# Kernel tuning notes

Hardware: AMD Instinct MI355X
Metric: run time of the kernel (lower is better)

The kernel has to match this reference:

```python
import jax, jax.numpy as jnp
import numpy as np

B, N, D_IN = 4, 2048, 1024
H, D_OUT = 8, 128


def setup_inputs() -> dict:
    key = jax.random.key(0)
    k1, k2, k3 = jax.random.split(key, 3)
    x = jax.random.normal(k1, (B, N, D_IN), dtype=jnp.float32)
    # W: (num_head, 3 [q,k,v], d_in, output_dim), glorot-ish scale
    W = jax.random.normal(k2, (H, 3, D_IN, D_OUT), dtype=jnp.float32) * (1.0 / np.sqrt(D_IN))
    Wo = jax.random.normal(k3, (H * D_OUT, D_OUT), dtype=jnp.float32) * (1.0 / np.sqrt(H * D_OUT))
    return {"x": x, "W": W, "Wo": Wo}


def reference(x, W, Wo):
    # Per-head QKV projections, vectorized over heads.
    # q,k,v: [B, H, N, D_OUT]
    q = jnp.einsum("bnd,hde->bhne", x, W[:, 0])
    k = jnp.einsum("bnd,hde->bhne", x, W[:, 1])
    v = jnp.einsum("bnd,hde->bhne", x, W[:, 2])
    scale = 1.0 / jnp.sqrt(jnp.asarray(D_OUT, dtype=x.dtype))
    # scores: [B, H, N, N]
    e = jnp.einsum("bhne,bhme->bhnm", q, k) * scale
    a = jax.nn.softmax(e, axis=-1)
    o = jnp.einsum("bhnm,bhme->bhne", a, v)  # [B, H, N, D_OUT]
    # concat heads -> [B, N, H*D_OUT]; head i occupies slice [i*D_OUT:(i+1)*D_OUT]
    o = jnp.transpose(o, (0, 2, 1, 3)).reshape(x.shape[0], x.shape[1], H * D_OUT)
    z = jnp.einsum("bnf,fe->bne", o, Wo)  # [B, N, D_OUT]
    return z
```

## Files before the change

### kernel.cpp

```cpp
#include <hip/hip_runtime.h>
#include <cstdint>


#define DEV __device__ __forceinline__

typedef _Float16 h8 __attribute__((ext_vector_type(8)));
typedef _Float16 h4 __attribute__((ext_vector_type(4)));
typedef float f4 __attribute__((ext_vector_type(4)));

typedef __attribute__((address_space(1))) const uint32_t gu32;
typedef __attribute__((address_space(3))) uint32_t lu32;

DEV float fexp2(float x) { return __builtin_amdgcn_exp2f(x); }

DEV f4 mfma16(h8 a, h8 b, f4 c) {
  return __builtin_amdgcn_mfma_f32_16x16x32_f16(a, b, c, 0, 0, 0);
}

DEV void g2l16(void* lds, const void* g) {
  __builtin_amdgcn_global_load_lds((gu32*)(uintptr_t)g, (lu32*)(uintptr_t)lds,
                                   16, 0, 0);
}

DEV f4 sx4(f4 v, int m) {
  f4 r;
  r[0] = __shfl_xor(v[0], m, 64);
  r[1] = __shfl_xor(v[1], m, 64);
  r[2] = __shfl_xor(v[2], m, 64);
  r[3] = __shfl_xor(v[3], m, 64);
  return r;
}

__global__ __launch_bounds__(256) void cvt_all_kernel(
    const float* __restrict__ x, _Float16* __restrict__ Xb,
    const float* __restrict__ W, const float* __restrict__ Wo,
    _Float16* __restrict__ WT, _Float16* __restrict__ WoT) {
  __shared__ float st[64][68];
  const int bid = blockIdx.x;
  const int tid = threadIdx.x;
  if (bid < 8192) {
    size_t i = (size_t)(bid * 256 + tid) * 4;
    f4 v = *(const f4*)(x + i);
    h4 o;
    o[0] = (_Float16)v[0];
    o[1] = (_Float16)v[1];
    o[2] = (_Float16)v[2];
    o[3] = (_Float16)v[3];
    *(h4*)(Xb + i) = o;
    return;
  }
  const int idx0 = bid - 8192;
  const int mz = idx0 >> 5;
  const int rem = idx0 & 31;
  const int d0 = (rem & 15) * 64;
  const int e0 = (rem >> 4) * 64;
  const float* src = (mz < 24) ? (W + (size_t)mz * 131072) : Wo;
  _Float16* dst = (mz < 24) ? (WT + (size_t)mz * 131072) : WoT;
#pragma unroll
  for (int r = 0; r < 4; ++r) {
    int idx = r * 256 + tid;
    int dd = idx >> 4, cc = (idx & 15) * 4;
    f4 v = *(const f4*)(src + (size_t)(d0 + dd) * 128 + e0 + cc);
    *(f4*)&st[dd][cc] = v;
  }
  __syncthreads();
#pragma unroll
  for (int r = 0; r < 2; ++r) {
    int idx = r * 256 + tid;
    int ee = idx >> 3, dd = (idx & 7) * 8;
    h8 o;
#pragma unroll
    for (int i = 0; i < 8; ++i) o[i] = (_Float16)st[dd + i][ee];
    *(h8*)(dst + (size_t)(e0 + ee) * 1024 + d0 + dd) = o;
  }
}

__global__ __launch_bounds__(256, 3) void gemm_qkv_kernel(
    const _Float16* __restrict__ A, const _Float16* __restrict__ BTall,
    _Float16* __restrict__ Qb, _Float16* __restrict__ Kb,
    _Float16* __restrict__ VTb) {
  constexpr int K = 1024;
  __shared__ __align__(16) _Float16 sAB[16384];
  const int tid = threadIdx.x;
  const int wave = tid >> 6, lane = tid & 63;
  const int g = lane >> 4, l15 = lane & 15;
  const int sw = l15 & 7;
  const int m0 = blockIdx.x * 128;
  const int j = blockIdx.y;
  const _Float16* BT = BTall + (size_t)j * (128 * 1024);

  f4 acc[4][4] = {};
  const int ar = (wave >> 1) * 64 + l15;
  const int br = (wave & 1) * 64 + l15;

#pragma unroll 1
  for (int kt = 0; kt < K; kt += 64) {
    __syncthreads();
#pragma unroll
    for (int r = 0; r < 4; ++r) {
      int idx = r * 256 + tid;
      int row = idx >> 3;
      int jg = (idx & 7) ^ (row & 7);
      g2l16(&sAB[idx * 8], A + (size_t)(m0 + row) * K + kt + jg * 8);
      g2l16(&sAB[8192 + idx * 8], BT + (size_t)row * K + kt + jg * 8);
    }
    __syncthreads();
#pragma unroll
    for (int ks = 0; ks < 2; ++ks) {
      int off = ((ks * 4 + g) ^ sw) * 8;
      h8 af[4], bf[4];
#pragma unroll
      for (int mt = 0; mt < 4; ++mt)
        af[mt] = *(const h8*)&sAB[(ar + mt * 16) * 64 + off];
#pragma unroll
      for (int nt = 0; nt < 4; ++nt)
        bf[nt] = *(const h8*)&sAB[8192 + (br + nt * 16) * 64 + off];
#pragma unroll
      for (int mt = 0; mt < 4; ++mt)
#pragma unroll
        for (int nt = 0; nt < 4; ++nt)
          acc[mt][nt] = mfma16(af[mt], bf[nt], acc[mt][nt]);
    }
  }

  const int wr = (wave >> 1) * 64, wc = (wave & 1) * 64;
  const int h = j / 3, s = j - h * 3;
  if (s < 2) {
    const float scl = (s == 0) ? 0.12751741032075984f : 1.0f;
    _Float16* dst = (s == 0) ? Qb : Kb;
    __syncthreads();
#pragma unroll
    for (int mt = 0; mt < 4; ++mt)
#pragma unroll
      for (int rg = 0; rg < 4; ++rg) {
        int rl = wr + mt * 16 + g * 4 + rg;
#pragma unroll
        for (int nt = 0; nt < 4; ++nt) {
          int c = wc + nt * 16 + l15;
          sAB[rl * 128 + (((c >> 3) ^ (rl & 7)) * 8) + (c & 7)] =
              (_Float16)(acc[mt][nt][rg] * scl);
        }
      }
    __syncthreads();
    int rr = tid >> 1, seg = tid & 1;
    int m = m0 + rr, b = m >> 11, n = m & 2047;
    size_t rb = ((size_t)((b * 8 + h) * 2048 + n)) * 128;
#pragma unroll
    for (int k = 0; k < 8; ++k) {
      int ch = seg * 8 + k;
      h8 v = *(const h8*)&sAB[rr * 128 + ((ch ^ (rr & 7)) * 8)];
      *(h8*)&dst[rb + ch * 8] = v;
    }
  } else {
    __syncthreads();
    const int b = m0 >> 11, n0 = m0 & 2047;
    size_t base = (size_t)(b * 8 + h) * (128 * 2048);
#pragma unroll
    for (int mt = 0; mt < 4; ++mt)
#pragma unroll
      for (int rg = 0; rg < 4; ++rg) {
        int nl = wr + mt * 16 + g * 4 + rg;
        int cc = (nl >> 3), ci = nl & 7;
#pragma unroll
        for (int nt = 0; nt < 4; ++nt) {
          int c = wc + nt * 16 + l15;
          sAB[c * 128 + ((cc ^ (c & 7)) * 8) + ci] = (_Float16)acc[mt][nt][rg];
        }
      }
    __syncthreads();
    int c = tid >> 1, seg = tid & 1;
#pragma unroll
    for (int k = 0; k < 8; ++k) {
      int ch = seg * 8 + k;
      h8 v = *(const h8*)&sAB[c * 128 + ((ch ^ (c & 7)) * 8)];
      *(h8*)&VTb[base + (size_t)c * 2048 + n0 + ch * 8] = v;
    }
  }
}

__global__ __launch_bounds__(512, 4) void flash_kernel(
    const _Float16* __restrict__ Qb, const _Float16* __restrict__ Kb,
    const _Float16* __restrict__ VTb, _Float16* __restrict__ Oc) {
  __shared__ __align__(16) _Float16 sK[64 * 128];
  __shared__ __align__(16) _Float16 sVT[128 * 64];
  __shared__ __align__(16) _Float16 sP[8 * 16 * 64];
  const int tid = threadIdx.x, wave = tid >> 6, lane = tid & 63;
  const int g = lane >> 4, l15 = lane & 15;
  const int sw = l15 & 7;
  const int bh = blockIdx.x, b = bh >> 3, h = bh & 7;
  const int q0 = blockIdx.y * 128;
  const _Float16* Q = Qb + (size_t)bh * (2048 * 128);
  const _Float16* Kp = Kb + (size_t)bh * (2048 * 128);
  const _Float16* VT = VTb + (size_t)bh * (128 * 2048);
  _Float16* sPw = &sP[wave * (16 * 64)];

  h8 qf[4];
#pragma unroll
  for (int kk = 0; kk < 4; ++kk)
    qf[kk] = *(const h8*)&Q[(size_t)(q0 + wave * 16 + l15) * 128 + kk * 32 + g * 8];

  f4 oacc[8] = {};
  f4 lstate = {};

#pragma unroll 1
  for (int kv0 = 0; kv0 < 2048; kv0 += 64) {
    __syncthreads();
#pragma unroll
    for (int r = 0; r < 2; ++r) {
      int idx = r * 512 + tid;
      int row = idx >> 4;
      int jg = (idx & 15) ^ (row & 7);
      g2l16(&sK[idx * 8], Kp + (size_t)(kv0 + row) * 128 + jg * 8);
      int row2 = idx >> 3;
      int jg2 = (idx & 7) ^ (row2 & 7);
      g2l16(&sVT[idx * 8], VT + (size_t)row2 * 2048 + kv0 + jg2 * 8);
    }
    __syncthreads();

    f4 sacc[4] = {};
#pragma unroll
    for (int kk = 0; kk < 4; ++kk) {
      int off = ((kk * 4 + g) ^ sw) * 8;
#pragma unroll
      for (int nt = 0; nt < 4; ++nt) {
        h8 bf = *(const h8*)&sK[(nt * 16 + l15) * 128 + off];
        sacc[nt] = mfma16(qf[kk], bf, sacc[nt]);
      }
    }

#pragma unroll
    for (int nt = 0; nt < 4; ++nt) {
      f4 p;
      p[0] = fexp2(sacc[nt][0]);
      p[1] = fexp2(sacc[nt][1]);
      p[2] = fexp2(sacc[nt][2]);
      p[3] = fexp2(sacc[nt][3]);
      lstate += p;
      int cc = nt * 2 + (l15 >> 3), ci = l15 & 7;
#pragma unroll
      for (int rg = 0; rg < 4; ++rg) {
        int rl = g * 4 + rg;
        sPw[rl * 64 + ((cc ^ (rl & 7)) * 8) + ci] = (_Float16)p[rg];
      }
    }

#pragma unroll
    for (int kk = 0; kk < 2; ++kk) {
      int off = ((kk * 4 + g) ^ sw) * 8;
      h8 pa = *(const h8*)&sPw[l15 * 64 + off];
#pragma unroll
      for (int nt = 0; nt < 8; ++nt) {
        h8 vb = *(const h8*)&sVT[(nt * 16 + l15) * 64 + off];
        oacc[nt] = mfma16(pa, vb, oacc[nt]);
      }
    }
  }

#pragma unroll
  for (int d = 1; d < 16; d <<= 1) lstate += sx4(lstate, d);
  f4 inv;
  inv[0] = 1.0f / lstate[0];
  inv[1] = 1.0f / lstate[1];
  inv[2] = 1.0f / lstate[2];
  inv[3] = 1.0f / lstate[3];
#pragma unroll
  for (int rg = 0; rg < 4; ++rg) {
    int n = q0 + wave * 16 + g * 4 + rg;
    size_t rb = ((size_t)(b * 2048 + n)) * 1024 + h * 128;
#pragma unroll
    for (int nt = 0; nt < 8; ++nt)
      Oc[rb + nt * 16 + l15] = (_Float16)(oacc[nt][rg] * inv[rg]);
  }
}

__global__ __launch_bounds__(256, 4) void gemm_out_kernel(
    const _Float16* __restrict__ A, const _Float16* __restrict__ BT,
    float* __restrict__ outF) {
  __shared__ __align__(16) _Float16 sA[16 * 64];
  __shared__ __align__(16) _Float16 sB[128 * 64];
  const int tid = threadIdx.x, wave = tid >> 6, lane = tid & 63;
  const int g = lane >> 4, l15 = lane & 15, sw = l15 & 7;
  const int m0 = blockIdx.x * 16;
  f4 acc[2] = {};

#pragma unroll 1
  for (int kt = 0; kt < 1024; kt += 64) {
    __syncthreads();
    if (tid < 128) {
      int row = tid >> 3;
      int jg = (tid & 7) ^ (row & 7);
      g2l16(&sA[tid * 8], A + (size_t)(m0 + row) * 1024 + kt + jg * 8);
    }
#pragma unroll
    for (int r = 0; r < 4; ++r) {
      int idx = r * 256 + tid;
      int row = idx >> 3;
      int jg = (idx & 7) ^ (row & 7);
      g2l16(&sB[idx * 8], BT + (size_t)row * 1024 + kt + jg * 8);
    }
    __syncthreads();
#pragma unroll
    for (int ks = 0; ks < 2; ++ks) {
      int off = ((ks * 4 + g) ^ sw) * 8;
      h8 af = *(const h8*)&sA[l15 * 64 + off];
#pragma unroll
      for (int nt = 0; nt < 2; ++nt) {
        h8 bf = *(const h8*)&sB[(wave * 32 + nt * 16 + l15) * 64 + off];
        acc[nt] = mfma16(af, bf, acc[nt]);
      }
    }
  }
#pragma unroll
  for (int rg = 0; rg < 4; ++rg) {
    int m = m0 + g * 4 + rg;
#pragma unroll
    for (int nt = 0; nt < 2; ++nt)
      outF[(size_t)m * 128 + wave * 32 + nt * 16 + l15] = acc[nt][rg];
  }
}

extern "C" void kernel_launch(void* const* d_in, const int* in_sizes, int n_in,
                              void* d_out, int out_size, void* d_ws,
                              size_t ws_size, hipStream_t stream) {
  const float* x = (const float*)d_in[0];
  const float* W = (const float*)d_in[1];
  const float* Wo = (const float*)d_in[2];
  float* out = (float*)d_out;
  char* ws = (char*)d_ws;

  _Float16* Xb = (_Float16*)(ws + 0);
  _Float16* WT = (_Float16*)(ws + 16777216);
  _Float16* WoT = (_Float16*)(ws + 23068672);
  _Float16* Qb = (_Float16*)(ws + 23330816);
  _Float16* Kb = (_Float16*)(ws + 40108032);
  _Float16* VTb = (_Float16*)(ws + 56885248);
  _Float16* Oc = (_Float16*)(ws + 73662464);

  cvt_all_kernel<<<8992, 256, 0, stream>>>(x, Xb, W, Wo, WT, WoT);
  gemm_qkv_kernel<<<dim3(64, 24), 256, 0, stream>>>(Xb, WT, Qb, Kb, VTb);
  flash_kernel<<<dim3(32, 16), 512, 0, stream>>>(Qb, Kb, VTb, Oc);
  gemm_out_kernel<<<512, 256, 0, stream>>>(Oc, WoT, out);
}
```

Before: 243.6 us.

## Rewrite flash attention with 32x32 MFMA, register-resident P, and double-buffered K/V

```diff
diff --git a/kernel.cpp b/kernel.cpp
--- a/kernel.cpp
+++ b/kernel.cpp
@@ -6,7 +6,11 @@
 
 typedef _Float16 h8 __attribute__((ext_vector_type(8)));
 typedef _Float16 h4 __attribute__((ext_vector_type(4)));
+typedef _Float16 h2 __attribute__((ext_vector_type(2)));
 typedef float f4 __attribute__((ext_vector_type(4)));
+typedef float f16x16 __attribute__((ext_vector_type(16)));
+typedef uint32_t u32x4 __attribute__((ext_vector_type(4)));
+typedef uint32_t u32x2 __attribute__((ext_vector_type(2)));
 
 typedef __attribute__((address_space(1))) const uint32_t gu32;
 typedef __attribute__((address_space(3))) uint32_t lu32;
@@ -15,6 +19,10 @@
 
 DEV f4 mfma16(h8 a, h8 b, f4 c) {
   return __builtin_amdgcn_mfma_f32_16x16x32_f16(a, b, c, 0, 0, 0);
+}
+
+DEV f16x16 mfma32(h8 a, h8 b, f16x16 c) {
+  return __builtin_amdgcn_mfma_f32_32x32x16_f16(a, b, c, 0, 0, 0);
 }
 
 DEV void g2l16(void* lds, const void* g) {
@@ -22,13 +30,15 @@
                                    16, 0, 0);
 }
 
-DEV f4 sx4(f4 v, int m) {
-  f4 r;
-  r[0] = __shfl_xor(v[0], m, 64);
-  r[1] = __shfl_xor(v[1], m, 64);
-  r[2] = __shfl_xor(v[2], m, 64);
-  r[3] = __shfl_xor(v[3], m, 64);
-  return r;
+DEV uint32_t pkrn(float a, float b) {
+  h2 t;
+  t[0] = (_Float16)a;
+  t[1] = (_Float16)b;
+  return __builtin_bit_cast(uint32_t, t);
+}
+
+DEV u32x2 pl32swap(uint32_t x, uint32_t y) {
+  return __builtin_amdgcn_permlane32_swap(x, y, false, false);
 }
 
 __global__ __launch_bounds__(256) void cvt_all_kernel(
@@ -178,98 +188,126 @@
   }
 }
 
-__global__ __launch_bounds__(512, 4) void flash_kernel(
+__global__ __launch_bounds__(256, 2) void flash_kernel(
     const _Float16* __restrict__ Qb, const _Float16* __restrict__ Kb,
     const _Float16* __restrict__ VTb, _Float16* __restrict__ Oc) {
-  __shared__ __align__(16) _Float16 sK[64 * 128];
-  __shared__ __align__(16) _Float16 sVT[128 * 64];
-  __shared__ __align__(16) _Float16 sP[8 * 16 * 64];
+  __shared__ __align__(16) _Float16 sK[2][64 * 128];
+  __shared__ __align__(16) _Float16 sVT[2][128 * 64];
   const int tid = threadIdx.x, wave = tid >> 6, lane = tid & 63;
-  const int g = lane >> 4, l15 = lane & 15;
-  const int sw = l15 & 7;
+  const int l31 = lane & 31, hi = lane >> 5;
+  const int sw = l31 & 7;
   const int bh = blockIdx.x, b = bh >> 3, h = bh & 7;
   const int q0 = blockIdx.y * 128;
   const _Float16* Q = Qb + (size_t)bh * (2048 * 128);
   const _Float16* Kp = Kb + (size_t)bh * (2048 * 128);
   const _Float16* VT = VTb + (size_t)bh * (128 * 2048);
-  _Float16* sPw = &sP[wave * (16 * 64)];
-
-  h8 qf[4];
-#pragma unroll
-  for (int kk = 0; kk < 4; ++kk)
-    qf[kk] = *(const h8*)&Q[(size_t)(q0 + wave * 16 + l15) * 128 + kk * 32 + g * 8];
-
-  f4 oacc[8] = {};
-  f4 lstate = {};
-
+
+  h8 qf[8];
+#pragma unroll
+  for (int c = 0; c < 8; ++c)
+    qf[c] = *(const h8*)&Q[(size_t)(q0 + wave * 32 + l31) * 128 + c * 16 +
+                           hi * 8];
+
+  f16x16 oacc[4] = {};
+  float lsum = 0.0f;
+
+#define STAGE(buf, kv0)                                                        \
+  {                                                                            \
+    _Float16* dK = &sK[buf][0];                                                \
+    _Float16* dV = &sVT[buf][0];                                               \
+    _Pragma("unroll") for (int i = 0; i < 4; ++i) {                            \
+      int idx = i * 256 + tid;                                                 \
+      int rk = idx >> 4, ck = idx & 15;                                        \
+      g2l16(dK + idx * 8,                                                      \
+            Kp + (size_t)((kv0) + rk) * 128 + ((ck ^ (rk & 7)) * 8));          \
+      int rv = idx >> 3, cv = idx & 7;                                         \
+      g2l16(dV + idx * 8,                                                      \
+            VT + (size_t)rv * 2048 + (kv0) + ((cv ^ (rv & 7)) * 8));           \
+    }                                                                          \
+  }
+
+  STAGE(0, 0);
+  int cur = 0;
 #pragma unroll 1
-  for (int kv0 = 0; kv0 < 2048; kv0 += 64) {
-    __syncthreads();
-#pragma unroll
-    for (int r = 0; r < 2; ++r) {
-      int idx = r * 512 + tid;
-      int row = idx >> 4;
-      int jg = (idx & 15) ^ (row & 7);
-      g2l16(&sK[idx * 8], Kp + (size_t)(kv0 + row) * 128 + jg * 8);
-      int row2 = idx >> 3;
-      int jg2 = (idx & 7) ^ (row2 & 7);
-      g2l16(&sVT[idx * 8], VT + (size_t)row2 * 2048 + kv0 + jg2 * 8);
-    }
-    __syncthreads();
-
-    f4 sacc[4] = {};
-#pragma unroll
-    for (int kk = 0; kk < 4; ++kk) {
-      int off = ((kk * 4 + g) ^ sw) * 8;
-#pragma unroll
-      for (int nt = 0; nt < 4; ++nt) {
-        h8 bf = *(const h8*)&sK[(nt * 16 + l15) * 128 + off];
-        sacc[nt] = mfma16(qf[kk], bf, sacc[nt]);
+  for (int t = 0; t < 32; ++t) {
+    __syncthreads();
+    if (t < 31) STAGE(cur ^ 1, (t + 1) * 64);
+    const _Float16* bK = &sK[cur][0];
+    const _Float16* bV = &sVT[cur][0];
+
+    f16x16 s0 = {}, s1 = {};
+#pragma unroll
+    for (int c = 0; c < 8; ++c) {
+      int off = ((c * 2 + hi) ^ sw) * 8;
+      h8 a0 = *(const h8*)&bK[l31 * 128 + off];
+      h8 a1 = *(const h8*)&bK[(32 + l31) * 128 + off];
+      s0 = mfma32(a0, qf[c], s0);
+      s1 = mfma32(a1, qf[c], s1);
+    }
+
+    uint32_t w0[8], w1[8];
+#pragma unroll
+    for (int j = 0; j < 8; ++j) {
+      float a0 = fexp2(s0[2 * j]), b0 = fexp2(s0[2 * j + 1]);
+      float a1 = fexp2(s1[2 * j]), b1 = fexp2(s1[2 * j + 1]);
+      lsum += (a0 + b0) + (a1 + b1);
+      w0[j] = pkrn(a0, b0);
+      w1[j] = pkrn(a1, b1);
+    }
+
+    h8 pf[4];
+#pragma unroll
+    for (int half = 0; half < 2; ++half) {
+      u32x2 r0 = pl32swap(w0[half * 4 + 0], w0[half * 4 + 2]);
+      u32x2 r1 = pl32swap(w0[half * 4 + 1], w0[half * 4 + 3]);
+      u32x4 tt;
+      tt[0] = r0[0];
+      tt[1] = r1[0];
+      tt[2] = r0[1];
+      tt[3] = r1[1];
+      pf[half] = __builtin_bit_cast(h8, tt);
+      u32x2 r2 = pl32swap(w1[half * 4 + 0], w1[half * 4 + 2]);
+      u32x2 r3 = pl32swap(w1[half * 4 + 1], w1[half * 4 + 3]);
+      u32x4 uu;
+      uu[0] = r2[0];
+      uu[1] = r3[0];
+      uu[2] = r2[1];
+      uu[3] = r3[1];
+      pf[2 + half] = __builtin_bit_cast(h8, uu);
+    }
+
+#pragma unroll
+    for (int dt = 0; dt < 4; ++dt) {
+#pragma unroll
+      for (int c = 0; c < 4; ++c) {
+        int off = ((c * 2 + hi) ^ sw) * 8;
+        h8 vf = *(const h8*)&bV[(dt * 32 + l31) * 64 + off];
+        oacc[dt] = mfma32(vf, pf[c], oacc[dt]);
       }
     }
-
-#pragma unroll
-    for (int nt = 0; nt < 4; ++nt) {
-      f4 p;
-      p[0] = fexp2(sacc[nt][0]);
-      p[1] = fexp2(sacc[nt][1]);
-      p[2] = fexp2(sacc[nt][2]);
-      p[3] = fexp2(sacc[nt][3]);
-      lstate += p;
-      int cc = nt * 2 + (l15 >> 3), ci = l15 & 7;
-#pragma unroll
-      for (int rg = 0; rg < 4; ++rg) {
-        int rl = g * 4 + rg;
-        sPw[rl * 64 + ((cc ^ (rl & 7)) * 8) + ci] = (_Float16)p[rg];
-      }
-    }
-
-#pragma unroll
-    for (int kk = 0; kk < 2; ++kk) {
-      int off = ((kk * 4 + g) ^ sw) * 8;
-      h8 pa = *(const h8*)&sPw[l15 * 64 + off];
-#pragma unroll
-      for (int nt = 0; nt < 8; ++nt) {
-        h8 vb = *(const h8*)&sVT[(nt * 16 + l15) * 64 + off];
-        oacc[nt] = mfma16(pa, vb, oacc[nt]);
-      }
-    }
-  }
-
-#pragma unroll
-  for (int d = 1; d < 16; d <<= 1) lstate += sx4(lstate, d);
-  f4 inv;
-  inv[0] = 1.0f / lstate[0];
-  inv[1] = 1.0f / lstate[1];
-  inv[2] = 1.0f / lstate[2];
-  inv[3] = 1.0f / lstate[3];
-#pragma unroll
-  for (int rg = 0; rg < 4; ++rg) {
-    int n = q0 + wave * 16 + g * 4 + rg;
-    size_t rb = ((size_t)(b * 2048 + n)) * 1024 + h * 128;
-#pragma unroll
-    for (int nt = 0; nt < 8; ++nt)
-      Oc[rb + nt * 16 + l15] = (_Float16)(oacc[nt][rg] * inv[rg]);
+    cur ^= 1;
+  }
+#undef STAGE
+
+  lsum += __shfl_xor(lsum, 32, 64);
+  const float inv = 1.0f / lsum;
+
+  __syncthreads();
+  _Float16* sO = &sK[0][0] + wave * 4096;
+#pragma unroll
+  for (int dt = 0; dt < 4; ++dt)
+#pragma unroll
+    for (int r = 0; r < 16; ++r) {
+      int d = dt * 32 + (r & 3) + 8 * (r >> 2) + 4 * hi;
+      sO[l31 * 128 + (d ^ (sw << 3))] = (_Float16)(oacc[dt][r] * inv);
+    }
+  const int l15 = lane & 15, gq = lane >> 4;
+#pragma unroll
+  for (int it = 0; it < 8; ++it) {
+    int q = it * 4 + gq;
+    h8 v = *(const h8*)&sO[q * 128 + ((l15 ^ (q & 7)) * 8)];
+    int n = q0 + wave * 32 + q;
+    *(h8*)&Oc[((size_t)(b * 2048 + n)) * 1024 + h * 128 + l15 * 8] = v;
   }
 }
 
@@ -338,6 +376,6 @@
 
   cvt_all_kernel<<<8992, 256, 0, stream>>>(x, Xb, W, Wo, WT, WoT);
   gemm_qkv_kernel<<<dim3(64, 24), 256, 0, stream>>>(Xb, WT, Qb, Kb, VTb);
-  flash_kernel<<<dim3(32, 16), 512, 0, stream>>>(Qb, Kb, VTb, Oc);
+  flash_kernel<<<dim3(32, 16), 256, 0, stream>>>(Qb, Kb, VTb, Oc);
   gemm_out_kernel<<<512, 256, 0, stream>>>(Oc, WoT, out);
 }
```

Result: no change. 241.5 us (-0.9%).
